# Optimization experiments

Hardware: AMD Instinct MI355X
Metric: run time of the kernel (lower is better)

## Reference

```python
import jax, jax.numpy as jnp
import numpy as np

B, N, C_IN, C_OUT, D, K = 64, 2048, 32, 32, 16, 2


def setup_inputs() -> dict:
    key = jax.random.key(0)
    k1, k2, k3, k4 = jax.random.split(key, 4)
    x = jax.random.normal(k1, (B, N, C_IN), dtype=jnp.float32)
    node_embeddings = jax.random.normal(k2, (N, D), dtype=jnp.float32)
    weights_pool = jax.random.normal(k3, (D, K, C_IN, C_OUT), dtype=jnp.float32)
    bias_pool = jax.random.normal(k4, (D, C_OUT), dtype=jnp.float32)
    return {"x": x, "node_embeddings": node_embeddings,
            "weights_pool": weights_pool, "bias_pool": bias_pool}


def reference(x, node_embeddings, weights_pool, bias_pool):
    n = node_embeddings.shape[0]
    # adaptive adjacency: softmax(relu(E E^T), axis=1)  [N, N]
    supports = jax.nn.softmax(jax.nn.relu(node_embeddings @ node_embeddings.T), axis=1)
    # stack [I, A]  -> [K=2, N, N]
    supports = jnp.stack([jnp.eye(n, dtype=supports.dtype), supports], axis=0)
    # per-node weights [N, K, C_in, C_out] and bias [N, C_out]
    weights = jnp.einsum('nd,dkio->nkio', node_embeddings, weights_pool)
    bias = node_embeddings @ bias_pool
    # graph aggregation: [K,N,N] x [B,N,C] -> [B,N,K,C]
    x_g = jnp.einsum('knm,bmc->bnkc', supports, x)
    # per-node batched small GEMM: [B,N,K,Ci] x [N,K,Ci,Co] -> [B,N,Co]
    x_gconv = jnp.einsum('bnki,nkio->bno', x_g, weights) + bias
    return x_gconv
```

## Files before the change

kernel.cpp:

```cpp
#include <hip/hip_runtime.h>


#define NN 2048
#define NB 64
#define CI 32
#define CO 32
#define DD 16

typedef _Float16 half8 __attribute__((ext_vector_type(8)));
typedef __attribute__((ext_vector_type(4))) float f32x4;

#define GLOAD16(gp, lp) __builtin_amdgcn_global_load_lds(                 \
    (const __attribute__((address_space(1))) void*)(gp),                  \
    (__attribute__((address_space(3))) void*)(lp), 16, 0, 0)

__global__ __launch_bounds__(256) void adjxT_kernel(const float* __restrict__ E,
                                                    const float* __restrict__ x,
                                                    _Float16* __restrict__ A,
                                                    _Float16* __restrict__ xT)
{
    const int n = blockIdx.x;
    const int tid = threadIdx.x;

    __shared__ float tile[64][33];
    __shared__ float row[NN];
    __shared__ float redmax[4];
    __shared__ float redsum[4];

    {
        const int b = n >> 5;
        const int m0 = (n & 31) * 64;
        #pragma unroll
        for (int k = 0; k < 2; ++k) {
            const int idx = tid + k * 256;
            const int r = idx >> 3, q = idx & 7;
            float4 v = *(const float4*)&x[((size_t)b * NN + m0 + r) * CI + q * 4];
            tile[r][q * 4 + 0] = v.x; tile[r][q * 4 + 1] = v.y;
            tile[r][q * 4 + 2] = v.z; tile[r][q * 4 + 3] = v.w;
        }
        __syncthreads();
        const int c = tid >> 3, m8 = (tid & 7) * 8;
        _Float16 o[8];
        #pragma unroll
        for (int e = 0; e < 8; ++e) o[e] = (_Float16)tile[m8 + e][c];
        *(uint4*)&xT[((size_t)b * CI + c) * NN + m0 + m8] = *(uint4*)o;
    }

    const float4* __restrict__ E4 = reinterpret_cast<const float4*>(E);
    const float4 e0 = E4[n * 4 + 0], e1 = E4[n * 4 + 1];
    const float4 e2 = E4[n * 4 + 2], e3 = E4[n * 4 + 3];

    float lmax = 0.0f;
    #pragma unroll
    for (int k = 0; k < NN / 256; ++k) {
        const int m = tid + k * 256;
        const float4 f0 = E4[m * 4 + 0], f1 = E4[m * 4 + 1];
        const float4 f2 = E4[m * 4 + 2], f3 = E4[m * 4 + 3];
        float dot = e0.x * f0.x + e0.y * f0.y + e0.z * f0.z + e0.w * f0.w;
        dot += e1.x * f1.x + e1.y * f1.y + e1.z * f1.z + e1.w * f1.w;
        dot += e2.x * f2.x + e2.y * f2.y + e2.z * f2.z + e2.w * f2.w;
        dot += e3.x * f3.x + e3.y * f3.y + e3.z * f3.z + e3.w * f3.w;
        dot = fmaxf(dot, 0.0f);
        row[m] = dot;
        lmax = fmaxf(lmax, dot);
    }
    #pragma unroll
    for (int off = 32; off > 0; off >>= 1)
        lmax = fmaxf(lmax, __shfl_down(lmax, off, 64));
    if ((tid & 63) == 0) redmax[tid >> 6] = lmax;
    __syncthreads();
    const float gmax = fmaxf(fmaxf(redmax[0], redmax[1]), fmaxf(redmax[2], redmax[3]));

    float lsum = 0.0f;
    #pragma unroll
    for (int k = 0; k < NN / 256; ++k) {
        const int m = tid + k * 256;
        const float v = __expf(row[m] - gmax);
        row[m] = v;
        lsum += v;
    }
    #pragma unroll
    for (int off = 32; off > 0; off >>= 1)
        lsum += __shfl_down(lsum, off, 64);
    if ((tid & 63) == 0) redsum[tid >> 6] = lsum;
    __syncthreads();
    const float inv = 1.0f / (redsum[0] + redsum[1] + redsum[2] + redsum[3]);

    #pragma unroll
    for (int k = 0; k < NN / 256; ++k) {
        const int m = tid + k * 256;
        A[(size_t)n * NN + m] = (_Float16)(row[m] * inv);
    }
}

__global__ __launch_bounds__(256, 2) void agg_mfma(const _Float16* __restrict__ A,
                                                   const _Float16* __restrict__ xT,
                                                   float* __restrict__ agg)
{
    const int wg = blockIdx.x;
    const int logical = (wg & 7) * 64 + (wg >> 3);
    const int jt = logical >> 5;
    const int nt = logical & 31;
    const int n0 = nt * 64;
    const int j0 = jt * 128;
    const int tid = threadIdx.x;
    const int lane = tid & 63;
    const int w = tid >> 6;
    const int wr = w >> 1, wc = w & 1;

    __shared__ __align__(16) unsigned char sm[49152];

    int soffA[2]; size_t gA[2];
    #pragma unroll
    for (int i = 0; i < 2; ++i) {
        const int off = i * 4096 + tid * 16;
        const int row = off >> 7, cb = off & 127;
        const int mm = (cb ^ ((row & 7) << 4)) >> 1;
        soffA[i] = off;
        gA[i] = (size_t)(n0 + row) * NN + mm;
    }
    int soffX[4]; size_t gX[4];
    #pragma unroll
    for (int i = 0; i < 4; ++i) {
        const int off = i * 4096 + tid * 16;
        const int row = off >> 7, cb = off & 127;
        const int mm = (cb ^ ((row & 7) << 4)) >> 1;
        soffX[i] = 8192 + off;
        gX[i] = (size_t)(j0 + row) * NN + mm;
    }

    const int l15 = lane & 15, lk = lane >> 4;
    const int sw = (lane & 7) << 4;
    int cbs[2];
    cbs[0] = (lk << 4) ^ sw;
    cbs[1] = (64 + (lk << 4)) ^ sw;
    int offA[2][2], offX[4][2];
    #pragma unroll
    for (int fm = 0; fm < 2; ++fm) {
        const int r = wr * 32 + fm * 16 + l15;
        #pragma unroll
        for (int s = 0; s < 2; ++s)
            offA[fm][s] = (r << 7) + cbs[s];
    }
    #pragma unroll
    for (int fj = 0; fj < 4; ++fj) {
        const int r = wc * 64 + fj * 16 + l15;
        #pragma unroll
        for (int s = 0; s < 2; ++s)
            offX[fj][s] = 8192 + (r << 7) + cbs[s];
    }

    f32x4 acc[2][4];
    #pragma unroll
    for (int fm = 0; fm < 2; ++fm)
        #pragma unroll
        for (int fj = 0; fj < 4; ++fj) acc[fm][fj] = (f32x4)0.0f;

    #pragma unroll
    for (int i = 0; i < 2; ++i)
        GLOAD16(A + gA[i], sm + soffA[i]);
    #pragma unroll
    for (int i = 0; i < 4; ++i)
        GLOAD16(xT + gX[i], sm + soffX[i]);
    __syncthreads();

    int buf = 0;
    for (int ks = 0; ks < NN / 64; ++ks) {
        const int nb = buf ^ 1;
        if (ks != NN / 64 - 1) {
            const size_t adv = (size_t)(ks + 1) * 64;
            #pragma unroll
            for (int i = 0; i < 2; ++i)
                GLOAD16(A + gA[i] + adv, sm + nb * 24576 + soffA[i]);
            #pragma unroll
            for (int i = 0; i < 4; ++i)
                GLOAD16(xT + gX[i] + adv, sm + nb * 24576 + soffX[i]);
        }
        const unsigned char* Bp = sm + buf * 24576;
        half8 av[2][2], xv[4][2];
        #pragma unroll
        for (int fm = 0; fm < 2; ++fm)
            #pragma unroll
            for (int s = 0; s < 2; ++s)
                av[fm][s] = *(const half8*)(Bp + offA[fm][s]);
        #pragma unroll
        for (int fj = 0; fj < 4; ++fj)
            #pragma unroll
            for (int s = 0; s < 2; ++s)
                xv[fj][s] = *(const half8*)(Bp + offX[fj][s]);

        #pragma unroll
        for (int s = 0; s < 2; ++s)
            #pragma unroll
            for (int fm = 0; fm < 2; ++fm)
                #pragma unroll
                for (int fj = 0; fj < 4; ++fj)
                    acc[fm][fj] = __builtin_amdgcn_mfma_f32_16x16x32_f16(
                        av[fm][s], xv[fj][s], acc[fm][fj], 0, 0, 0);
        __syncthreads();
        buf = nb;
    }

    #pragma unroll
    for (int fm = 0; fm < 2; ++fm)
        #pragma unroll
        for (int fj = 0; fj < 4; ++fj) {
            const int nbase = n0 + wr * 32 + fm * 16 + lk * 4;
            const int j = j0 + wc * 64 + fj * 16 + l15;
            const int b = j >> 5, c = j & 31;
            #pragma unroll
            for (int r = 0; r < 4; ++r)
                agg[((size_t)b * NN + nbase + r) * CI + c] = acc[fm][fj][r];
        }
}

__global__ __launch_bounds__(256) void outw_kernel(const float* __restrict__ E,
                                                   const float* __restrict__ Wp,
                                                   const float* __restrict__ Bp,
                                                   const float* __restrict__ x,
                                                   float* __restrict__ out)
{
    const int n = blockIdx.x;
    const int tid = threadIdx.x;

    __shared__ __align__(16) float W[2 * CI * CO];
    __shared__ __align__(16) float Xs[NB][CI];
    __shared__ __align__(16) float Gs[NB][CI];

    {
        const int b = tid >> 3, q = (tid & 7) * 4;
        const int b2 = (tid + 256) >> 3;
        GLOAD16(x + ((size_t)b * NN + n) * CI + q,     (char*)Xs + tid * 16);
        GLOAD16(x + ((size_t)b2 * NN + n) * CI + q,    (char*)Xs + 4096 + tid * 16);
        GLOAD16(out + ((size_t)b * NN + n) * CI + q,   (char*)Gs + tid * 16);
        GLOAD16(out + ((size_t)b2 * NN + n) * CI + q,  (char*)Gs + 4096 + tid * 16);
    }

    float e[DD];
    #pragma unroll
    for (int d = 0; d < DD; ++d) e[d] = E[n * DD + d];

    {
        const float4* __restrict__ Wp4 = (const float4*)Wp;
        float4 a0 = make_float4(0.f, 0.f, 0.f, 0.f);
        float4 a1 = make_float4(0.f, 0.f, 0.f, 0.f);
        #pragma unroll
        for (int d = 0; d < DD; ++d) {
            const float4 w0 = Wp4[d * 512 + tid];
            const float4 w1 = Wp4[d * 512 + 256 + tid];
            const float c = e[d];
            a0.x = fmaf(c, w0.x, a0.x); a0.y = fmaf(c, w0.y, a0.y);
            a0.z = fmaf(c, w0.z, a0.z); a0.w = fmaf(c, w0.w, a0.w);
            a1.x = fmaf(c, w1.x, a1.x); a1.y = fmaf(c, w1.y, a1.y);
            a1.z = fmaf(c, w1.z, a1.z); a1.w = fmaf(c, w1.w, a1.w);
        }
        *(float4*)&W[tid * 4] = a0;
        *(float4*)&W[1024 + tid * 4] = a1;
    }
    __syncthreads();

    const int o  = tid & 31;
    const int bb = tid >> 5;

    float bias = 0.0f;
    #pragma unroll
    for (int d = 0; d < DD; ++d) bias = fmaf(e[d], Bp[d * CO + o], bias);

    float w0[CI], w1[CI];
    #pragma unroll
    for (int i = 0; i < CI; ++i) {
        w0[i] = W[i * 32 + o];
        w1[i] = W[1024 + i * 32 + o];
    }

    #pragma unroll
    for (int j = 0; j < 8; ++j) {
        const int b = bb + 8 * j;
        float s = bias;
        #pragma unroll
        for (int iq = 0; iq < 8; ++iq) {
            const float4 xq = *(const float4*)&Xs[b][iq * 4];
            const float4 gq = *(const float4*)&Gs[b][iq * 4];
            s = fmaf(xq.x, w0[iq * 4 + 0], s);
            s = fmaf(xq.y, w0[iq * 4 + 1], s);
            s = fmaf(xq.z, w0[iq * 4 + 2], s);
            s = fmaf(xq.w, w0[iq * 4 + 3], s);
            s = fmaf(gq.x, w1[iq * 4 + 0], s);
            s = fmaf(gq.y, w1[iq * 4 + 1], s);
            s = fmaf(gq.z, w1[iq * 4 + 2], s);
            s = fmaf(gq.w, w1[iq * 4 + 3], s);
        }
        out[((size_t)b * NN + n) * CO + o] = s;
    }
}

extern "C" void kernel_launch(void* const* d_in, const int* in_sizes, int n_in,
                              void* d_out, int out_size, void* d_ws, size_t ws_size,
                              hipStream_t stream)
{
    const float* x  = (const float*)d_in[0];
    const float* E  = (const float*)d_in[1];
    const float* Wp = (const float*)d_in[2];
    const float* Bp = (const float*)d_in[3];
    float* out = (float*)d_out;

    _Float16* A  = (_Float16*)d_ws;
    _Float16* xT = A + (size_t)NN * NN;

    adjxT_kernel<<<NN, 256, 0, stream>>>(E, x, A, xT);
    agg_mfma<<<512, 256, 0, stream>>>(A, xT, out);
    outw_kernel<<<NN, 256, 0, stream>>>(E, Wp, Bp, x, out);
}
```

Measured before the change: 137.8 us.

## Fuse three kernels into one cooperative kernel with grid syncs

Merges the adjacency/transpose, MFMA aggregation GEMM and per-node output stages into a single cooperative kernel of 512 blocks separated by grid.sync, with each block handling four rows in the first and last stages. The goal is to remove the launch gaps and tail effects between the three separate kernel launches. In exchange, the first and last stages run at reduced parallelism (512 blocks instead of 2048), and each grid-wide barrier adds its own cost. If the cooperative launch fails, the code falls back to the original three launches.

```diff
diff --git a/kernel.cpp b/kernel.cpp
--- a/kernel.cpp
+++ b/kernel.cpp
@@ -1,4 +1,7 @@
 #include <hip/hip_runtime.h>
+#include <hip/hip_cooperative_groups.h>
+
+namespace cg = cooperative_groups;
 
 
 #define NN 2048
@@ -14,45 +17,18 @@
     (const __attribute__((address_space(1))) void*)(gp),                  \
     (__attribute__((address_space(3))) void*)(lp), 16, 0, 0)
 
-__global__ __launch_bounds__(256) void adjxT_kernel(const float* __restrict__ E,
-                                                    const float* __restrict__ x,
-                                                    _Float16* __restrict__ A,
-                                                    _Float16* __restrict__ xT)
-{
-    const int n = blockIdx.x;
-    const int tid = threadIdx.x;
-
-    __shared__ float tile[64][33];
-    __shared__ float row[NN];
-    __shared__ float redmax[4];
-    __shared__ float redsum[4];
-
-    {
-        const int b = n >> 5;
-        const int m0 = (n & 31) * 64;
-        #pragma unroll
-        for (int k = 0; k < 2; ++k) {
-            const int idx = tid + k * 256;
-            const int r = idx >> 3, q = idx & 7;
-            float4 v = *(const float4*)&x[((size_t)b * NN + m0 + r) * CI + q * 4];
-            tile[r][q * 4 + 0] = v.x; tile[r][q * 4 + 1] = v.y;
-            tile[r][q * 4 + 2] = v.z; tile[r][q * 4 + 3] = v.w;
-        }
-        __syncthreads();
-        const int c = tid >> 3, m8 = (tid & 7) * 8;
-        _Float16 o[8];
-        #pragma unroll
-        for (int e = 0; e < 8; ++e) o[e] = (_Float16)tile[m8 + e][c];
-        *(uint4*)&xT[((size_t)b * CI + c) * NN + m0 + m8] = *(uint4*)o;
-    }
-
-    const float4* __restrict__ E4 = reinterpret_cast<const float4*>(E);
+
+__device__ __forceinline__ void adj_row_body(const float* __restrict__ E,
+                                             _Float16* __restrict__ A,
+                                             float* row, float* redmax,
+                                             float* redsum, int n, int tid)
+{
+    const float4* __restrict__ E4 = (const float4*)E;
     const float4 e0 = E4[n * 4 + 0], e1 = E4[n * 4 + 1];
     const float4 e2 = E4[n * 4 + 2], e3 = E4[n * 4 + 3];
-
     float lmax = 0.0f;
     #pragma unroll
-    for (int k = 0; k < NN / 256; ++k) {
+    for (int k = 0; k < 8; ++k) {
         const int m = tid + k * 256;
         const float4 f0 = E4[m * 4 + 0], f1 = E4[m * 4 + 1];
         const float4 f2 = E4[m * 4 + 2], f3 = E4[m * 4 + 3];
@@ -69,11 +45,11 @@
         lmax = fmaxf(lmax, __shfl_down(lmax, off, 64));
     if ((tid & 63) == 0) redmax[tid >> 6] = lmax;
     __syncthreads();
-    const float gmax = fmaxf(fmaxf(redmax[0], redmax[1]), fmaxf(redmax[2], redmax[3]));
-
+    const float gmax = fmaxf(fmaxf(redmax[0], redmax[1]),
+                             fmaxf(redmax[2], redmax[3]));
     float lsum = 0.0f;
     #pragma unroll
-    for (int k = 0; k < NN / 256; ++k) {
+    for (int k = 0; k < 8; ++k) {
         const int m = tid + k * 256;
         const float v = __expf(row[m] - gmax);
         row[m] = v;
@@ -85,30 +61,43 @@
     if ((tid & 63) == 0) redsum[tid >> 6] = lsum;
     __syncthreads();
     const float inv = 1.0f / (redsum[0] + redsum[1] + redsum[2] + redsum[3]);
-
-    #pragma unroll
-    for (int k = 0; k < NN / 256; ++k) {
+    #pragma unroll
+    for (int k = 0; k < 8; ++k) {
         const int m = tid + k * 256;
         A[(size_t)n * NN + m] = (_Float16)(row[m] * inv);
     }
 }
 
-__global__ __launch_bounds__(256, 2) void agg_mfma(const _Float16* __restrict__ A,
-                                                   const _Float16* __restrict__ xT,
-                                                   float* __restrict__ agg)
-{
-    const int wg = blockIdx.x;
-    const int logical = (wg & 7) * 64 + (wg >> 3);
-    const int jt = logical >> 5;
-    const int nt = logical & 31;
-    const int n0 = nt * 64;
-    const int j0 = jt * 128;
-    const int tid = threadIdx.x;
+__device__ __forceinline__ void xT_tile_body(const float* __restrict__ x,
+                                             _Float16* __restrict__ xT,
+                                             float (*tile)[33], int n, int tid)
+{
+    const int b = n >> 5, m0 = (n & 31) * 64;
+    #pragma unroll
+    for (int k = 0; k < 2; ++k) {
+        const int idx = tid + k * 256;
+        const int rr = idx >> 3, q = idx & 7;
+        float4 v = *(const float4*)&x[((size_t)b * NN + m0 + rr) * CI + q * 4];
+        tile[rr][q * 4 + 0] = v.x; tile[rr][q * 4 + 1] = v.y;
+        tile[rr][q * 4 + 2] = v.z; tile[rr][q * 4 + 3] = v.w;
+    }
+    __syncthreads();
+    const int c = tid >> 3, m8 = (tid & 7) * 8;
+    _Float16 o[8];
+    #pragma unroll
+    for (int e = 0; e < 8; ++e) o[e] = (_Float16)tile[m8 + e][c];
+    *(uint4*)&xT[((size_t)b * CI + c) * NN + m0 + m8] = *(uint4*)o;
+}
+
+__device__ __forceinline__ void gemm_tile_body(const _Float16* __restrict__ A,
+                                               const _Float16* __restrict__ xT,
+                                               float* __restrict__ agg,
+                                               unsigned char* sm,
+                                               int n0, int j0, int tid)
+{
     const int lane = tid & 63;
     const int w = tid >> 6;
     const int wr = w >> 1, wc = w & 1;
-
-    __shared__ __align__(16) unsigned char sm[49152];
 
     int soffA[2]; size_t gA[2];
     #pragma unroll
@@ -137,17 +126,17 @@
     int offA[2][2], offX[4][2];
     #pragma unroll
     for (int fm = 0; fm < 2; ++fm) {
-        const int r = wr * 32 + fm * 16 + l15;
+        const int rr = wr * 32 + fm * 16 + l15;
         #pragma unroll
         for (int s = 0; s < 2; ++s)
-            offA[fm][s] = (r << 7) + cbs[s];
+            offA[fm][s] = (rr << 7) + cbs[s];
     }
     #pragma unroll
     for (int fj = 0; fj < 4; ++fj) {
-        const int r = wc * 64 + fj * 16 + l15;
+        const int rr = wc * 64 + fj * 16 + l15;
         #pragma unroll
         for (int s = 0; s < 2; ++s)
-            offX[fj][s] = 8192 + (r << 7) + cbs[s];
+            offX[fj][s] = 8192 + (rr << 7) + cbs[s];
     }
 
     f32x4 acc[2][4];
@@ -176,18 +165,18 @@
             for (int i = 0; i < 4; ++i)
                 GLOAD16(xT + gX[i] + adv, sm + nb * 24576 + soffX[i]);
         }
-        const unsigned char* Bp = sm + buf * 24576;
+        const unsigned char* Bp2 = sm + buf * 24576;
         half8 av[2][2], xv[4][2];
         #pragma unroll
         for (int fm = 0; fm < 2; ++fm)
             #pragma unroll
             for (int s = 0; s < 2; ++s)
-                av[fm][s] = *(const half8*)(Bp + offA[fm][s]);
+                av[fm][s] = *(const half8*)(Bp2 + offA[fm][s]);
         #pragma unroll
         for (int fj = 0; fj < 4; ++fj)
             #pragma unroll
             for (int s = 0; s < 2; ++s)
-                xv[fj][s] = *(const half8*)(Bp + offX[fj][s]);
+                xv[fj][s] = *(const half8*)(Bp2 + offX[fj][s]);
 
         #pragma unroll
         for (int s = 0; s < 2; ++s)
@@ -209,31 +198,26 @@
             const int j = j0 + wc * 64 + fj * 16 + l15;
             const int b = j >> 5, c = j & 31;
             #pragma unroll
-            for (int r = 0; r < 4; ++r)
-                agg[((size_t)b * NN + nbase + r) * CI + c] = acc[fm][fj][r];
-        }
-}
-
-__global__ __launch_bounds__(256) void outw_kernel(const float* __restrict__ E,
-                                                   const float* __restrict__ Wp,
-                                                   const float* __restrict__ Bp,
-                                                   const float* __restrict__ x,
-                                                   float* __restrict__ out)
-{
-    const int n = blockIdx.x;
-    const int tid = threadIdx.x;
-
-    __shared__ __align__(16) float W[2 * CI * CO];
-    __shared__ __align__(16) float Xs[NB][CI];
-    __shared__ __align__(16) float Gs[NB][CI];
-
+            for (int rr = 0; rr < 4; ++rr)
+                agg[((size_t)b * NN + nbase + rr) * CI + c] = acc[fm][fj][rr];
+        }
+}
+
+__device__ __forceinline__ void outw_body(const float* __restrict__ E,
+                                          const float* __restrict__ Wp,
+                                          const float* __restrict__ Bp,
+                                          const float* __restrict__ x,
+                                          float* __restrict__ out,
+                                          float* W, float (*Xs)[CI],
+                                          float (*Gs)[CI], int n, int tid)
+{
     {
         const int b = tid >> 3, q = (tid & 7) * 4;
         const int b2 = (tid + 256) >> 3;
-        GLOAD16(x + ((size_t)b * NN + n) * CI + q,     (char*)Xs + tid * 16);
-        GLOAD16(x + ((size_t)b2 * NN + n) * CI + q,    (char*)Xs + 4096 + tid * 16);
-        GLOAD16(out + ((size_t)b * NN + n) * CI + q,   (char*)Gs + tid * 16);
-        GLOAD16(out + ((size_t)b2 * NN + n) * CI + q,  (char*)Gs + 4096 + tid * 16);
+        GLOAD16(x + ((size_t)b * NN + n) * CI + q,    (char*)Xs + tid * 16);
+        GLOAD16(x + ((size_t)b2 * NN + n) * CI + q,   (char*)Xs + 4096 + tid * 16);
+        GLOAD16(out + ((size_t)b * NN + n) * CI + q,  (char*)Gs + tid * 16);
+        GLOAD16(out + ((size_t)b2 * NN + n) * CI + q, (char*)Gs + 4096 + tid * 16);
     }
 
     float e[DD];
@@ -246,13 +230,13 @@
         float4 a1 = make_float4(0.f, 0.f, 0.f, 0.f);
         #pragma unroll
         for (int d = 0; d < DD; ++d) {
-            const float4 w0 = Wp4[d * 512 + tid];
-            const float4 w1 = Wp4[d * 512 + 256 + tid];
+            const float4 w0v = Wp4[d * 512 + tid];
+            const float4 w1v = Wp4[d * 512 + 256 + tid];
             const float c = e[d];
-            a0.x = fmaf(c, w0.x, a0.x); a0.y = fmaf(c, w0.y, a0.y);
-            a0.z = fmaf(c, w0.z, a0.z); a0.w = fmaf(c, w0.w, a0.w);
-            a1.x = fmaf(c, w1.x, a1.x); a1.y = fmaf(c, w1.y, a1.y);
-            a1.z = fmaf(c, w1.z, a1.z); a1.w = fmaf(c, w1.w, a1.w);
+            a0.x = fmaf(c, w0v.x, a0.x); a0.y = fmaf(c, w0v.y, a0.y);
+            a0.z = fmaf(c, w0v.z, a0.z); a0.w = fmaf(c, w0v.w, a0.w);
+            a1.x = fmaf(c, w1v.x, a1.x); a1.y = fmaf(c, w1v.y, a1.y);
+            a1.z = fmaf(c, w1v.z, a1.z); a1.w = fmaf(c, w1v.w, a1.w);
         }
         *(float4*)&W[tid * 4] = a0;
         *(float4*)&W[1024 + tid * 4] = a1;
@@ -294,6 +278,90 @@
     }
 }
 
+
+__global__ __launch_bounds__(256) void adjxT_kernel(const float* __restrict__ E,
+                                                    const float* __restrict__ x,
+                                                    _Float16* __restrict__ A,
+                                                    _Float16* __restrict__ xT)
+{
+    __shared__ float tile[64][33];
+    __shared__ float row[NN];
+    __shared__ float redmax[4];
+    __shared__ float redsum[4];
+    xT_tile_body(x, xT, tile, blockIdx.x, threadIdx.x);
+    adj_row_body(E, A, row, redmax, redsum, blockIdx.x, threadIdx.x);
+}
+
+__global__ __launch_bounds__(256, 2) void agg_mfma(const _Float16* __restrict__ A,
+                                                   const _Float16* __restrict__ xT,
+                                                   float* __restrict__ agg)
+{
+    const int wg = blockIdx.x;
+    const int logical = (wg & 7) * 64 + (wg >> 3);
+    __shared__ __align__(16) unsigned char sm[49152];
+    gemm_tile_body(A, xT, agg, sm, (logical & 31) * 64, (logical >> 5) * 128,
+                   threadIdx.x);
+}
+
+__global__ __launch_bounds__(256) void outw_kernel(const float* __restrict__ E,
+                                                   const float* __restrict__ Wp,
+                                                   const float* __restrict__ Bp,
+                                                   const float* __restrict__ x,
+                                                   float* __restrict__ out)
+{
+    __shared__ __align__(16) float W[2 * CI * CO];
+    __shared__ __align__(16) float Xs[NB][CI];
+    __shared__ __align__(16) float Gs[NB][CI];
+    outw_body(E, Wp, Bp, x, out, W, Xs, Gs, blockIdx.x, threadIdx.x);
+}
+
+
+__global__ __launch_bounds__(256, 2) void fused_kernel(
+    const float* __restrict__ E, const float* __restrict__ x,
+    const float* __restrict__ Wp, const float* __restrict__ Bp,
+    float* __restrict__ out, _Float16* __restrict__ A,
+    _Float16* __restrict__ xT)
+{
+    cg::grid_group grid = cg::this_grid();
+    const int tid = threadIdx.x;
+    const int blk = blockIdx.x;
+
+    __shared__ __align__(16) unsigned char sm[49152];
+
+    {
+        float* row = (float*)sm;
+        float (*tile)[33] = (float(*)[33])(sm + 8192);
+        float* redmax = (float*)(sm + 16640);
+        float* redsum = (float*)(sm + 16656);
+        for (int r = 0; r < 4; ++r) {
+            const int n = blk * 4 + r;
+            xT_tile_body(x, xT, tile, n, tid);
+            adj_row_body(E, A, row, redmax, redsum, n, tid);
+            __syncthreads();
+        }
+    }
+    __threadfence();
+    grid.sync();
+
+    {
+        const int logical = (blk & 7) * 64 + (blk >> 3);
+        gemm_tile_body(A, xT, out, sm, (logical & 31) * 64,
+                       (logical >> 5) * 128, tid);
+    }
+    __threadfence();
+    grid.sync();
+
+    {
+        float* W = (float*)sm;
+        float (*Xs)[CI] = (float(*)[CI])(sm + 8192);
+        float (*Gs)[CI] = (float(*)[CI])(sm + 16384);
+        for (int r = 0; r < 4; ++r) {
+            outw_body(E, Wp, Bp, x, out, W, Xs, Gs, blk * 4 + r, tid);
+            __syncthreads();
+        }
+    }
+}
+
 extern "C" void kernel_launch(void* const* d_in, const int* in_sizes, int n_in,
                               void* d_out, int out_size, void* d_ws, size_t ws_size,
                               hipStream_t stream)
@@ -307,7 +375,14 @@
     _Float16* A  = (_Float16*)d_ws;
     _Float16* xT = A + (size_t)NN * NN;
 
-    adjxT_kernel<<<NN, 256, 0, stream>>>(E, x, A, xT);
-    agg_mfma<<<512, 256, 0, stream>>>(A, xT, out);
-    outw_kernel<<<NN, 256, 0, stream>>>(E, Wp, Bp, x, out);
-}
+    void* args[] = {(void*)&E, (void*)&x, (void*)&Wp, (void*)&Bp,
+                    (void*)&out, (void*)&A, (void*)&xT};
+    hipError_t err = hipLaunchCooperativeKernel((void*)fused_kernel, dim3(512),
+                                                dim3(256), args, 0, stream);
+    if (err != hipSuccess) {
+        (void)hipGetLastError();
+        adjxT_kernel<<<NN, 256, 0, stream>>>(E, x, A, xT);
+        agg_mfma<<<512, 256, 0, stream>>>(A, xT, out);
+        outw_kernel<<<NN, 256, 0, stream>>>(E, Wp, Bp, x, out);
+    }
+}
```

New measurement: 345.7 us. +150.9%, slower.
